# Kernel optimization log

Measured on AMD Instinct MI355X. Metric: run time of the kernel, lower is better.

The kernel has to match this reference:

```python
import jax, jax.numpy as jnp
import numpy as np

EPS = 1e-6

def setup_inputs() -> dict:
    key = jax.random.key(0)
    k1, k2, k3 = jax.random.split(key, 3)
    D = 1024
    return {
        "x": jax.random.normal(k1, (2, 2048, D), dtype=jnp.float32),
        "w_norm": jnp.ones((D,), dtype=jnp.float32),
        "w_qkv": jax.random.normal(k2, (3 * D, D), dtype=jnp.float32) * (1.0 / np.sqrt(D)),
        "w_out": jax.random.normal(k3, (D, D), dtype=jnp.float32) * (1.0 / np.sqrt(D)),
        "window_size": 128,
        "n_heads": 16,
    }

def reference(x, w_norm, w_qkv, w_out, window_size, n_heads):
    B, L, D = x.shape
    H = n_heads
    dh = D // H
    skip = x
    # RMSNorm
    rms = jnp.sqrt(jnp.mean(x * x, axis=-1, keepdims=True) + EPS)
    xn = w_norm * (x / rms)
    # QKV projection (torch Linear: y = x @ W.T)
    qkv = xn @ w_qkv.T  # [B, L, 3D]
    q, k, v = jnp.split(qkv, 3, axis=-1)
    q = q.reshape(B, L, H, dh).transpose(0, 2, 1, 3)  # [B,H,L,dh]
    k = k.reshape(B, L, H, dh).transpose(0, 2, 1, 3)
    v = v.reshape(B, L, H, dh).transpose(0, 2, 1, 3)
    scores = jnp.einsum("bhid,bhjd->bhij", q, k) / np.sqrt(dh)  # [B,H,L,L]
    # Symmetric window: token i attends to j in [i - w//2, i + w//2]
    idx = jnp.arange(L)
    half = window_size // 2
    band = jnp.abs(idx[:, None] - idx[None, :]) <= half  # [L, L]
    scores = jnp.where(band, scores, -jnp.inf)
    attn = jax.nn.softmax(scores, axis=-1)  # zeros outside band, matches torch loop
    out = jnp.einsum("bhij,bhjd->bhid", attn, v)  # [B,H,L,dh]
    out = out.transpose(0, 2, 1, 3).reshape(B, L, D)
    out = out @ w_out.T
    return out + skip
```

## Files before the change

kernel.cpp:

```cpp
#include <hip/hip_runtime.h>
#include <hip/hip_bf16.h>
#include <cstdint>

typedef float f32x4 __attribute__((ext_vector_type(4)));
typedef short s16x8 __attribute__((ext_vector_type(8)));

constexpr int B_ = 2, L_ = 2048, D_ = 1024, H_ = 16, DH = 64, HALF = 64;
constexpr int M_ROWS = B_ * L_;
constexpr int QKV_N = 3 * D_;

__device__ __forceinline__ void gload16(const void* g, void* l) {
    __builtin_amdgcn_global_load_lds(
        (const __attribute__((address_space(1))) unsigned int*)g,
        (__attribute__((address_space(3))) unsigned int*)l, 16, 0, 0);
}

__global__ void rmsnorm_kernel(const float* __restrict__ x, const float* __restrict__ wn,
                               __hip_bfloat16* __restrict__ xn) {
    int row = blockIdx.x;
    int t = threadIdx.x;
    const float4* xr = reinterpret_cast<const float4*>(x + (size_t)row * D_);
    float4 v = xr[t];
    float ss = v.x * v.x + v.y * v.y + v.z * v.z + v.w * v.w;
#pragma unroll
    for (int off = 32; off; off >>= 1) ss += __shfl_xor(ss, off);
    __shared__ float red[4];
    if ((t & 63) == 0) red[t >> 6] = ss;
    __syncthreads();
    float tot = red[0] + red[1] + red[2] + red[3];
    float rinv = rsqrtf(tot * (1.0f / D_) + 1e-6f);
    const float4* wr = reinterpret_cast<const float4*>(wn);
    float4 w = wr[t];
    __hip_bfloat16* o = xn + (size_t)row * D_ + t * 4;
    o[0] = __float2bfloat16(v.x * rinv * w.x);
    o[1] = __float2bfloat16(v.y * rinv * w.y);
    o[2] = __float2bfloat16(v.z * rinv * w.z);
    o[3] = __float2bfloat16(v.w * rinv * w.w);
}

__global__ void cvt_weights_kernel(const float* __restrict__ wq, const float* __restrict__ wo,
                                   __hip_bfloat16* __restrict__ oq, __hip_bfloat16* __restrict__ oo) {
    constexpr int NQ4 = QKV_N * D_ / 4;
    int i = blockIdx.x * blockDim.x + threadIdx.x;
    const float* src; __hip_bfloat16* dst; int j;
    if (i < NQ4) { src = wq; dst = oq; j = i; }
    else         { src = wo; dst = oo; j = i - NQ4; }
    float4 v = reinterpret_cast<const float4*>(src)[j];
    __hip_bfloat16* o = dst + (size_t)j * 4;
    o[0] = __float2bfloat16(v.x);
    o[1] = __float2bfloat16(v.y);
    o[2] = __float2bfloat16(v.z);
    o[3] = __float2bfloat16(v.w);
}

template <int EPI>
__global__ __launch_bounds__(256, 2) void gemm_pipe_kernel(const __hip_bfloat16* __restrict__ A,
                                                           const __hip_bfloat16* __restrict__ Bt,
                                                           __hip_bfloat16* __restrict__ Cbf,
                                                           float* __restrict__ Cf,
                                                           const float* __restrict__ resid,
                                                           int M, int N, int K) {
    constexpr int BM = 128, BN = 128;
    constexpr int BUF = (BM + BN) * 128;
    __shared__ __align__(16) char smem[2 * BUF];

    const int tid = threadIdx.x;
    const int lane = tid & 63;
    const int wid = tid >> 6;

    int nwg = gridDim.x * gridDim.y;
    int lin = blockIdx.y * gridDim.x + blockIdx.x;
    int cpx = nwg >> 3;
    int swz = (lin & 7) * cpx + (lin >> 3);
    int bx = swz % gridDim.x;
    int by = swz / gridDim.x;

    const int rowBase = by * BM;
    const int colBase = bx * BN;
    const int NTILES = K >> 6;

    const int srow = tid >> 3;
    const int colSw = ((tid & 7) ^ (srow & 7)) << 3;
    const __hip_bfloat16* aG = A + (size_t)(rowBase + srow) * K + colSw;
    const __hip_bfloat16* bG = Bt + (size_t)(colBase + srow) * K + colSw;
    const int dstW = wid << 10;

    const int wm = wid >> 1, wn = wid & 1;
    const int l15 = lane & 15, hi = lane >> 4;
    const int s7 = l15 & 7;
    const int rA = wm * 64 + l15;
    const int rB = wn * 64 + l15;

    f32x4 acc[4][4];
#pragma unroll
    for (int m = 0; m < 4; ++m)
#pragma unroll
        for (int n = 0; n < 4; ++n) acc[m][n] = (f32x4){0.f, 0.f, 0.f, 0.f};

    {
        const __hip_bfloat16* as = aG;
        const __hip_bfloat16* bs = bG;
#pragma unroll
        for (int i = 0; i < 4; ++i) {
            gload16(as + (size_t)(i * 32) * K, smem + i * 4096 + dstW);
            gload16(bs + (size_t)(i * 32) * K, smem + BM * 128 + i * 4096 + dstW);
        }
    }

    for (int kt = 0; kt < NTILES; ++kt) {
        const int bf = kt & 1;
        __builtin_amdgcn_s_barrier();
        if (kt + 1 < NTILES) {
            char* base = smem + (bf ^ 1) * BUF;
            const __hip_bfloat16* as = aG + (size_t)(kt + 1) * 64;
            const __hip_bfloat16* bs = bG + (size_t)(kt + 1) * 64;
#pragma unroll
            for (int i = 0; i < 4; ++i) {
                gload16(as + (size_t)(i * 32) * K, base + i * 4096 + dstW);
                gload16(bs + (size_t)(i * 32) * K, base + BM * 128 + i * 4096 + dstW);
            }
            asm volatile("s_waitcnt vmcnt(8)" ::: "memory");
        } else {
            asm volatile("s_waitcnt vmcnt(0)" ::: "memory");
        }

        const char* ab = smem + bf * BUF;
        const char* bb = ab + BM * 128;
        s16x8 af[4][2], bfr[4][2];
#pragma unroll
        for (int mf = 0; mf < 4; ++mf)
#pragma unroll
            for (int kk = 0; kk < 2; ++kk)
                af[mf][kk] = *(const s16x8*)(ab + (rA + mf * 16) * 128 + (((kk * 4 + hi) ^ s7) << 4));
#pragma unroll
        for (int nf = 0; nf < 4; ++nf)
#pragma unroll
            for (int kk = 0; kk < 2; ++kk)
                bfr[nf][kk] = *(const s16x8*)(bb + (rB + nf * 16) * 128 + (((kk * 4 + hi) ^ s7) << 4));

        __builtin_amdgcn_s_setprio(1);
#pragma unroll
        for (int kk = 0; kk < 2; ++kk)
#pragma unroll
            for (int mf = 0; mf < 4; ++mf)
#pragma unroll
                for (int nf = 0; nf < 4; ++nf)
                    acc[mf][nf] = __builtin_amdgcn_mfma_f32_16x16x32_bf16(af[mf][kk], bfr[nf][kk],
                                                                          acc[mf][nf], 0, 0, 0);
        __builtin_amdgcn_s_setprio(0);
    }

#pragma unroll
    for (int mf = 0; mf < 4; ++mf) {
#pragma unroll
        for (int nf = 0; nf < 4; ++nf) {
            int col = colBase + wn * 64 + nf * 16 + l15;
#pragma unroll
            for (int r = 0; r < 4; ++r) {
                int row = rowBase + wm * 64 + mf * 16 + 4 * hi + r;
                if (EPI == 0) {
                    Cbf[(size_t)row * N + col] = __float2bfloat16(acc[mf][nf][r]);
                } else {
                    Cf[(size_t)row * N + col] = acc[mf][nf][r] + resid[(size_t)row * N + col];
                }
            }
        }
    }
}

__global__ __launch_bounds__(128) void attn_mfma_kernel(const __hip_bfloat16* __restrict__ qkv,
                                                        __hip_bfloat16* __restrict__ attn) {
    __shared__ __align__(16) char smem[50176];
    constexpr int VT_OFF = 24576;
    int tid = threadIdx.x;
    int tq = blockIdx.x, h = blockIdx.y, b = blockIdx.z;
    int q0 = tq * 64;
    int jg0 = q0 - HALF;
    const __hip_bfloat16* qkvb = qkv + (size_t)(b * L_) * QKV_N;

    {
        int r8 = tid >> 3, cs = tid & 7;
        short* Vt = (short*)(smem + VT_OFF);
#pragma unroll
        for (int seg = 0; seg < 12; ++seg) {
            int row = r8 + seg * 16;
            int jg = jg0 + row;
            int jc = jg < 0 ? 0 : (jg > L_ - 1 ? L_ - 1 : jg);
            const short* src = (const short*)(qkvb + (size_t)jc * QKV_N + D_ + h * DH + cs * 8);
            s16x8 kv = *(const s16x8*)src;
            int slot = cs ^ (row & 7);
            *(s16x8*)(smem + row * 128 + slot * 16) = kv;
            s16x8 vv = *(const s16x8*)(src + D_);
#pragma unroll
            for (int e = 0; e < 8; ++e)
                Vt[(cs * 8 + e) * 200 + row] = vv[e];
        }
    }
    __syncthreads();

    int lane = tid & 63, w = tid >> 6;
    int l15 = lane & 15, hi = lane >> 4;

    s16x8 aq[2][2];
#pragma unroll
    for (int m = 0; m < 2; ++m)
#pragma unroll
        for (int kk = 0; kk < 2; ++kk)
            aq[m][kk] = *(const s16x8*)(qkvb + (size_t)(q0 + 32 * w + 16 * m + l15) * QKV_N
                                        + h * DH + kk * 32 + hi * 8);

    f32x4 sc[2][10];
#pragma unroll
    for (int m = 0; m < 2; ++m)
#pragma unroll
        for (int kt = 0; kt < 10; ++kt) sc[m][kt] = (f32x4){0.f, 0.f, 0.f, 0.f};

#pragma unroll
    for (int kt = 0; kt < 10; ++kt) {
        int jl = 32 * w + 16 * kt + l15;
        s16x8 bk0 = *(const s16x8*)(smem + jl * 128 + ((hi ^ (jl & 7)) * 16));
        s16x8 bk1 = *(const s16x8*)(smem + jl * 128 + (((4 + hi) ^ (jl & 7)) * 16));
#pragma unroll
        for (int m = 0; m < 2; ++m) {
            sc[m][kt] = __builtin_amdgcn_mfma_f32_16x16x32_bf16(aq[m][0], bk0, sc[m][kt], 0, 0, 0);
            sc[m][kt] = __builtin_amdgcn_mfma_f32_16x16x32_bf16(aq[m][1], bk1, sc[m][kt], 0, 0, 0);
        }
    }

#pragma unroll
    for (int m = 0; m < 2; ++m) {
#pragma unroll
        for (int r = 0; r < 4; ++r) {
            int iloc = 32 * w + 16 * m + 4 * hi + r;
            float mx = -1e30f;
#pragma unroll
            for (int kt = 0; kt < 10; ++kt) {
                int jl = 32 * w + 16 * kt + l15;
                int jg = jg0 + jl;
                bool ok = (jl >= iloc) && (jl <= iloc + 2 * HALF) && (jg >= 0) && (jg < L_);
                float s = ok ? sc[m][kt][r] * 0.125f : -1e30f;
                sc[m][kt][r] = s;
                mx = fmaxf(mx, s);
            }
            mx = fmaxf(mx, __shfl_xor(mx, 1));
            mx = fmaxf(mx, __shfl_xor(mx, 2));
            mx = fmaxf(mx, __shfl_xor(mx, 4));
            mx = fmaxf(mx, __shfl_xor(mx, 8));
            float sum = 0.f;
#pragma unroll
            for (int kt = 0; kt < 10; ++kt) {
                float p = __expf(sc[m][kt][r] - mx);
                sc[m][kt][r] = p;
                sum += p;
            }
            sum += __shfl_xor(sum, 1);
            sum += __shfl_xor(sum, 2);
            sum += __shfl_xor(sum, 4);
            sum += __shfl_xor(sum, 8);
            float inv = 1.0f / sum;
#pragma unroll
            for (int kt = 0; kt < 10; ++kt) sc[m][kt][r] *= inv;
        }
    }

    __syncthreads();

    {
        __hip_bfloat16* Pw = (__hip_bfloat16*)(smem + w * 10752);
#pragma unroll
        for (int m = 0; m < 2; ++m)
#pragma unroll
            for (int kt = 0; kt < 10; ++kt)
#pragma unroll
                for (int r = 0; r < 4; ++r)
                    Pw[(16 * m + 4 * hi + r) * 168 + 16 * kt + l15] = __float2bfloat16(sc[m][kt][r]);
    }
    __syncthreads();

    f32x4 o[2][4];
#pragma unroll
    for (int m = 0; m < 2; ++m)
#pragma unroll
        for (int nt = 0; nt < 4; ++nt) o[m][nt] = (f32x4){0.f, 0.f, 0.f, 0.f};

#pragma unroll
    for (int kst = 0; kst < 5; ++kst) {
        s16x8 ap[2];
#pragma unroll
        for (int m = 0; m < 2; ++m)
            ap[m] = *(const s16x8*)(smem + w * 10752 + (16 * m + l15) * 336 + (32 * kst + 8 * hi) * 2);
#pragma unroll
        for (int nt = 0; nt < 4; ++nt) {
            s16x8 bv = *(const s16x8*)(smem + VT_OFF + (16 * nt + l15) * 400
                                       + (32 * w + 32 * kst + 8 * hi) * 2);
#pragma unroll
            for (int m = 0; m < 2; ++m)
                o[m][nt] = __builtin_amdgcn_mfma_f32_16x16x32_bf16(ap[m], bv, o[m][nt], 0, 0, 0);
        }
    }

#pragma unroll
    for (int m = 0; m < 2; ++m)
#pragma unroll
        for (int nt = 0; nt < 4; ++nt)
#pragma unroll
            for (int r = 0; r < 4; ++r) {
                int rowg = q0 + 32 * w + 16 * m + 4 * hi + r;
                attn[(size_t)(b * L_ + rowg) * D_ + h * DH + 16 * nt + l15] =
                    __float2bfloat16(o[m][nt][r]);
            }
}

extern "C" void kernel_launch(void* const* d_in, const int* in_sizes, int n_in,
                              void* d_out, int out_size, void* d_ws, size_t ws_size,
                              hipStream_t stream) {
    const float* x      = (const float*)d_in[0];
    const float* w_norm = (const float*)d_in[1];
    const float* w_qkv  = (const float*)d_in[2];
    const float* w_out  = (const float*)d_in[3];

    char* ws = (char*)d_ws;
    __hip_bfloat16* xn   = (__hip_bfloat16*)(ws);
    __hip_bfloat16* wq   = (__hip_bfloat16*)(ws + (8u  << 20));
    __hip_bfloat16* wo   = (__hip_bfloat16*)(ws + (14u << 20));
    __hip_bfloat16* qkv  = (__hip_bfloat16*)(ws + (16u << 20));
    __hip_bfloat16* attn = (__hip_bfloat16*)(ws + (40u << 20));
    float* out = (float*)d_out;

    {
        int n4 = (QKV_N * D_ + D_ * D_) / 4;
        cvt_weights_kernel<<<n4 / 256, 256, 0, stream>>>(w_qkv, w_out, wq, wo);
    }

    rmsnorm_kernel<<<M_ROWS, 256, 0, stream>>>(x, w_norm, xn);

    gemm_pipe_kernel<0><<<dim3(QKV_N / 128, M_ROWS / 128), 256, 0, stream>>>(
        xn, wq, qkv, nullptr, nullptr, M_ROWS, QKV_N, D_);

    attn_mfma_kernel<<<dim3(L_ / 64, H_, B_), 128, 0, stream>>>(qkv, attn);

    gemm_pipe_kernel<1><<<dim3(D_ / 128, M_ROWS / 128), 256, 0, stream>>>(
        attn, wo, nullptr, out, x, M_ROWS, D_, D_);
}
```

Before: 91.88 us.

## Write V transposed from QKV GEMM epilogue and DMA K/V tiles into LDS

The QKV GEMM epilogue now writes the V third of its output into a separate per-head transposed buffer [B,H,dh,L] using packed 4-element stores. The attention kernel then loads both K and this transposed V straight into LDS with async global_load_lds, using XOR-swizzled layouts. This removes the scalar per-element LDS transpose of V inside the attention kernel. The cost is an extra workspace buffer and a more complex GEMM epilogue, and edge clamping of V is done at 8-token granularity.

```diff
diff --git a/kernel.cpp b/kernel.cpp
--- a/kernel.cpp
+++ b/kernel.cpp
@@ -4,6 +4,7 @@
 
 typedef float f32x4 __attribute__((ext_vector_type(4)));
 typedef short s16x8 __attribute__((ext_vector_type(8)));
+typedef short s16x4 __attribute__((ext_vector_type(4)));
 
 constexpr int B_ = 2, L_ = 2048, D_ = 1024, H_ = 16, DH = 64, HALF = 64;
 constexpr int M_ROWS = B_ * L_;
@@ -57,6 +58,7 @@
 __global__ __launch_bounds__(256, 2) void gemm_pipe_kernel(const __hip_bfloat16* __restrict__ A,
                                                            const __hip_bfloat16* __restrict__ Bt,
                                                            __hip_bfloat16* __restrict__ Cbf,
+                                                           __hip_bfloat16* __restrict__ vT,
                                                            float* __restrict__ Cf,
                                                            const float* __restrict__ resid,
                                                            int M, int N, int K) {
@@ -97,14 +99,10 @@
 #pragma unroll
         for (int n = 0; n < 4; ++n) acc[m][n] = (f32x4){0.f, 0.f, 0.f, 0.f};
 
-    {
-        const __hip_bfloat16* as = aG;
-        const __hip_bfloat16* bs = bG;
-#pragma unroll
-        for (int i = 0; i < 4; ++i) {
-            gload16(as + (size_t)(i * 32) * K, smem + i * 4096 + dstW);
-            gload16(bs + (size_t)(i * 32) * K, smem + BM * 128 + i * 4096 + dstW);
-        }
+#pragma unroll
+    for (int i = 0; i < 4; ++i) {
+        gload16(aG + (size_t)(i * 32) * K, smem + i * 4096 + dstW);
+        gload16(bG + (size_t)(i * 32) * K, smem + BM * 128 + i * 4096 + dstW);
     }
 
     for (int kt = 0; kt < NTILES; ++kt) {
@@ -155,50 +153,68 @@
 #pragma unroll
         for (int nf = 0; nf < 4; ++nf) {
             int col = colBase + wn * 64 + nf * 16 + l15;
-#pragma unroll
-            for (int r = 0; r < 4; ++r) {
-                int row = rowBase + wm * 64 + mf * 16 + 4 * hi + r;
-                if (EPI == 0) {
-                    Cbf[(size_t)row * N + col] = __float2bfloat16(acc[mf][nf][r]);
+            int row0 = rowBase + wm * 64 + mf * 16 + 4 * hi;
+            if (EPI == 0) {
+                if (col < 2 * D_) {
+#pragma unroll
+                    for (int r = 0; r < 4; ++r)
+                        Cbf[(size_t)(row0 + r) * N + col] = __float2bfloat16(acc[mf][nf][r]);
                 } else {
-                    Cf[(size_t)row * N + col] = acc[mf][nf][r] + resid[(size_t)row * N + col];
+                    int h = (col - 2 * D_) >> 6;
+                    int dim = (col - 2 * D_) & 63;
+                    int bb2 = row0 >> 11, i0 = row0 & (L_ - 1);
+                    s16x4 pk;
+#pragma unroll
+                    for (int r = 0; r < 4; ++r) {
+                        __hip_bfloat16 t = __float2bfloat16(acc[mf][nf][r]);
+                        pk[r] = *reinterpret_cast<short*>(&t);
+                    }
+                    *(s16x4*)(vT + ((size_t)(bb2 * H_ + h) * DH + dim) * L_ + i0) = pk;
                 }
+            } else {
+#pragma unroll
+                for (int r = 0; r < 4; ++r)
+                    Cf[(size_t)(row0 + r) * N + col] = acc[mf][nf][r] + resid[(size_t)(row0 + r) * N + col];
             }
         }
     }
 }
 
 __global__ __launch_bounds__(128) void attn_mfma_kernel(const __hip_bfloat16* __restrict__ qkv,
+                                                        const __hip_bfloat16* __restrict__ vT,
                                                         __hip_bfloat16* __restrict__ attn) {
-    __shared__ __align__(16) char smem[50176];
-    constexpr int VT_OFF = 24576;
+    __shared__ __align__(16) char smem[57344];
+    constexpr int VOFF = 24576;
     int tid = threadIdx.x;
+    int lane = tid & 63, w = tid >> 6;
     int tq = blockIdx.x, h = blockIdx.y, b = blockIdx.z;
     int q0 = tq * 64;
     int jg0 = q0 - HALF;
     const __hip_bfloat16* qkvb = qkv + (size_t)(b * L_) * QKV_N;
-
-    {
-        int r8 = tid >> 3, cs = tid & 7;
-        short* Vt = (short*)(smem + VT_OFF);
-#pragma unroll
-        for (int seg = 0; seg < 12; ++seg) {
-            int row = r8 + seg * 16;
-            int jg = jg0 + row;
-            int jc = jg < 0 ? 0 : (jg > L_ - 1 ? L_ - 1 : jg);
-            const short* src = (const short*)(qkvb + (size_t)jc * QKV_N + D_ + h * DH + cs * 8);
-            s16x8 kv = *(const s16x8*)src;
-            int slot = cs ^ (row & 7);
-            *(s16x8*)(smem + row * 128 + slot * 16) = kv;
-            s16x8 vv = *(const s16x8*)(src + D_);
-#pragma unroll
-            for (int e = 0; e < 8; ++e)
-                Vt[(cs * 8 + e) * 200 + row] = vv[e];
-        }
+    const __hip_bfloat16* vTg = vT + (size_t)(b * H_ + h) * DH * L_;
+
+#pragma unroll
+    for (int it = 0; it < 12; ++it) {
+        int ob = (it * 2 + w) << 10;
+        int o = ob + lane * 16;
+        int row = o >> 7;
+        int c = ((o >> 4) & 7) ^ (row & 7);
+        int jg = jg0 + row;
+        int jc = jg < 0 ? 0 : (jg > L_ - 1 ? L_ - 1 : jg);
+        gload16(qkvb + (size_t)jc * QKV_N + D_ + h * DH + c * 8, smem + ob);
+    }
+#pragma unroll
+    for (int it = 0; it < 16; ++it) {
+        int ob = (it * 2 + w) << 10;
+        int o = ob + lane * 16;
+        int d = o >> 9;
+        int c = ((o >> 4) & 31) ^ (d & 7);
+        int kb = jg0 + c * 8;
+        int kc = kb < 0 ? 0 : (kb > L_ - 8 ? L_ - 8 : kb);
+        gload16(vTg + (size_t)d * L_ + kc, smem + VOFF + ob);
     }
     __syncthreads();
 
-    int lane = tid & 63, w = tid >> 6;
     int l15 = lane & 15, hi = lane >> 4;
 
     s16x8 aq[2][2];
@@ -291,8 +307,9 @@
             ap[m] = *(const s16x8*)(smem + w * 10752 + (16 * m + l15) * 336 + (32 * kst + 8 * hi) * 2);
 #pragma unroll
         for (int nt = 0; nt < 4; ++nt) {
-            s16x8 bv = *(const s16x8*)(smem + VT_OFF + (16 * nt + l15) * 400
-                                       + (32 * w + 32 * kst + 8 * hi) * 2);
+            int d = 16 * nt + l15;
+            int c = 4 * w + 4 * kst + hi;
+            s16x8 bv = *(const s16x8*)(smem + VOFF + d * 512 + ((c ^ (d & 7)) << 4));
 #pragma unroll
             for (int m = 0; m < 2; ++m)
                 o[m][nt] = __builtin_amdgcn_mfma_f32_16x16x32_bf16(ap[m], bv, o[m][nt], 0, 0, 0);
@@ -325,6 +342,7 @@
     __hip_bfloat16* wo   = (__hip_bfloat16*)(ws + (14u << 20));
     __hip_bfloat16* qkv  = (__hip_bfloat16*)(ws + (16u << 20));
     __hip_bfloat16* attn = (__hip_bfloat16*)(ws + (40u << 20));
+    __hip_bfloat16* vT   = (__hip_bfloat16*)(ws + (48u << 20));
     float* out = (float*)d_out;
 
     {
@@ -335,10 +353,10 @@
     rmsnorm_kernel<<<M_ROWS, 256, 0, stream>>>(x, w_norm, xn);
 
     gemm_pipe_kernel<0><<<dim3(QKV_N / 128, M_ROWS / 128), 256, 0, stream>>>(
-        xn, wq, qkv, nullptr, nullptr, M_ROWS, QKV_N, D_);
-
-    attn_mfma_kernel<<<dim3(L_ / 64, H_, B_), 128, 0, stream>>>(qkv, attn);
+        xn, wq, qkv, vT, nullptr, nullptr, M_ROWS, QKV_N, D_);
+
+    attn_mfma_kernel<<<dim3(L_ / 64, H_, B_), 128, 0, stream>>>(qkv, vT, attn);
 
     gemm_pipe_kernel<1><<<dim3(D_ / 128, M_ROWS / 128), 256, 0, stream>>>(
-        attn, wo, nullptr, out, x, M_ROWS, D_, D_);
-}
+        attn, wo, nullptr, nullptr, out, x, M_ROWS, D_, D_);
+}
```

New measurement: 93.34 us. No clear change (+1.6%).
